# Kernel tuning notes

Hardware: AMD Instinct MI355X
Metric: run time of the kernel (lower is better)

The kernel has to match this reference:

```python
import jax, jax.numpy as jnp
import numpy as np

N_NODES = 50000
N_EDGES = 800000
D_FEAT = 64
NEG_SLOPE = 0.01  # nn.LeakyReLU default


def setup_inputs() -> dict:
    key = jax.random.key(0)
    ks = jax.random.split(key, 8)
    in_feat = jax.random.normal(ks[0], (N_NODES, D_FEAT), dtype=jnp.float32)
    src = jax.random.randint(ks[1], (N_EDGES,), 0, N_NODES, dtype=jnp.int64)
    dst = jax.random.randint(ks[2], (N_EDGES,), 0, N_NODES, dtype=jnp.int64)
    scale = 1.0 / np.sqrt(D_FEAT)
    W1 = jax.random.normal(ks[3], (D_FEAT, D_FEAT), dtype=jnp.float32) * scale
    b1 = jnp.zeros((D_FEAT,), dtype=jnp.float32)
    W2 = jax.random.normal(ks[4], (D_FEAT, D_FEAT), dtype=jnp.float32) * scale
    b2 = jnp.zeros((D_FEAT,), dtype=jnp.float32)
    return {"in_feat": in_feat, "W1": W1, "b1": b1, "W2": W2, "b2": b2,
            "src": src, "dst": dst}


def reference(in_feat, W1, b1, W2, b2, src, dst):
    # Eval-mode GCN: Dropout and DropEdge are identity; per-layer the graph
    # has its self-loops removed (mask src==dst edges) and one canonical
    # self-loop per node re-added. GraphConv uses norm='both':
    #   out = LeakyReLU( (D_in^{-1/2} A D_out^{-1/2} X) W + b )
    N = in_feat.shape[0]
    mask = (src != dst).astype(in_feat.dtype)  # remove_self_loop
    # degrees including the single added self-loop
    out_deg = jax.ops.segment_sum(mask, src, num_segments=N) + 1.0
    in_deg = jax.ops.segment_sum(mask, dst, num_segments=N) + 1.0
    inv_out = jax.lax.rsqrt(out_deg)[:, None]  # [N,1]
    inv_in = jax.lax.rsqrt(in_deg)[:, None]

    def layer(h, W, b):
        hs = h * inv_out                                   # src-side norm
        msg = hs[src] * mask[:, None]                      # gather, drop self-loops
        agg = jax.ops.segment_sum(msg, dst, num_segments=N) + hs  # + self-loop
        agg = agg * inv_in                                 # dst-side norm
        return jax.nn.leaky_relu(agg @ W + b, negative_slope=NEG_SLOPE)

    h = layer(in_feat, W1, b1)
    h = layer(h, W2, b2)
    return h
```

## Files before the change

kernel.cpp:

```cpp
#include <hip/hip_runtime.h>
#include <hip/hip_fp16.h>
#include <stdint.h>

#define D 64
#define NEG_SLOPE 0.01f
#define CAP 64


__global__ void k_zero(int* p, int n) {
    int i = blockIdx.x * blockDim.x + threadIdx.x;
    if (i < n) p[i] = 0;
}

__global__ void k_build(const int* __restrict__ src, const int* __restrict__ dst,
                        int* __restrict__ cnt_in, int* __restrict__ cnt_out,
                        int* __restrict__ colp, int E) {
    int e = blockIdx.x * blockDim.x + threadIdx.x;
    if (e >= E) return;
    int s = src[e], d = dst[e];
    if (s != d) {
        int r = atomicAdd(&cnt_in[d], 1);
        if (r < CAP) colp[(d << 6) + r] = s;
        atomicAdd(&cnt_out[s], 1);
    }
}

__global__ void k_inv(const int* __restrict__ cnt, float* __restrict__ inv, int n2) {
    int i = blockIdx.x * blockDim.x + threadIdx.x;
    if (i < n2) inv[i] = rsqrtf((float)cnt[i] + 1.0f);
}

__global__ void k_prescale(const float* __restrict__ x, const float* __restrict__ inv,
                           __half* __restrict__ y, int total4) {
    int i = blockIdx.x * blockDim.x + threadIdx.x;
    if (i >= total4) return;
    float4 v = reinterpret_cast<const float4*>(x)[i];
    float s = inv[i >> 4];
    __half2* yo = reinterpret_cast<__half2*>(y) + 2 * (size_t)i;
    yo[0] = __half2{__float2half_rn(v.x * s), __float2half_rn(v.y * s)};
    yo[1] = __half2{__float2half_rn(v.z * s), __float2half_rn(v.w * s)};
}

template <bool WRITE_HALF>
__global__ __launch_bounds__(256, 2)
void k_layer(const int* __restrict__ cnt_in, const int* __restrict__ colp,
             const __half* __restrict__ h,
             const float* __restrict__ inv_out, const float* __restrict__ inv_in,
             const float* __restrict__ W, const float* __restrict__ b,
             void* __restrict__ out_, int N) {
    __shared__ float Ws[D * D];
    int tid = threadIdx.x;
    {
        const float4* W4 = reinterpret_cast<const float4*>(W);
        float4* Ws4 = reinterpret_cast<float4*>(Ws);
        for (int i = tid; i < D * D / 4; i += 256) Ws4[i] = W4[i];
    }
    __syncthreads();

    const int lane = tid & 63;
    const int s = lane >> 4;
    const int g = lane & 15;
    const int subbase = lane & 48;
    const int nwaves = gridDim.x * (256 >> 6);
    const int wave0 = (blockIdx.x * 256 + tid) >> 6;
    const int ngroups = (N + 3) >> 2;

    for (int grp = wave0; grp < ngroups; grp += nwaves) {
        const int base = grp * 4;
        const int node = base + s;
        const bool nvalid = node < N;

        int dg = 0;
        if (lane < 4 && base + lane < N) dg = cnt_in[base + lane];
        int deg = __shfl(dg, s);
        deg = deg > CAP ? CAP : deg;
        if (!nvalid) deg = 0;

        int dmax = max(deg, __shfl_xor(deg, 16));
        dmax = max(dmax, __shfl_xor(dmax, 32));

        float a0 = 0.f, a1 = 0.f, a2 = 0.f, a3 = 0.f;
        const int cbase = node << 6;

        for (int cb = 0; cb < dmax; cb += 16) {
            int cnt = deg - cb;  cnt = cnt < 0 ? 0 : (cnt > 16 ? 16 : cnt);
            int cmax = dmax - cb; cmax = cmax > 16 ? 16 : cmax;
            int ci = (g < cnt) ? colp[cbase + cb + g] : 0;
            #pragma unroll
            for (int half = 0; half < 2; ++half) {
                if (half * 8 >= cmax) break;
                uint2 v[8];
                float m[8];
                #pragma unroll
                for (int q = 0; q < 8; ++q) {
                    int it = half * 8 + q;
                    int sn = __shfl(ci, subbase | it);
                    m[q] = (it < cnt) ? 1.f : 0.f;
                    v[q] = *reinterpret_cast<const uint2*>(h + (size_t)sn * D + g * 4);
                }
                #pragma unroll
                for (int q = 0; q < 8; ++q) {
                    float2 f0 = __half22float2(*reinterpret_cast<const __half2*>(&v[q].x));
                    float2 f1 = __half22float2(*reinterpret_cast<const __half2*>(&v[q].y));
                    a0 = fmaf(m[q], f0.x, a0); a1 = fmaf(m[q], f0.y, a1);
                    a2 = fmaf(m[q], f1.x, a2); a3 = fmaf(m[q], f1.y, a3);
                }
            }
        }

        const int nn = nvalid ? node : 0;
        {
            uint2 u = *reinterpret_cast<const uint2*>(h + (size_t)nn * D + g * 4);
            float2 f0 = __half22float2(*reinterpret_cast<const __half2*>(&u.x));
            float2 f1 = __half22float2(*reinterpret_cast<const __half2*>(&u.y));
            float m = nvalid ? 1.f : 0.f;
            a0 = fmaf(m, f0.x, a0); a1 = fmaf(m, f0.y, a1);
            a2 = fmaf(m, f1.x, a2); a3 = fmaf(m, f1.y, a3);
        }
        const float sc = inv_in[nn];
        a0 *= sc; a1 *= sc; a2 *= sc; a3 *= sc;

        const float4 bb = reinterpret_cast<const float4*>(b)[g];
        float r0 = bb.x, r1 = bb.y, r2 = bb.z, r3 = bb.w;
        #pragma unroll
        for (int kq = 0; kq < 16; ++kq) {
            int srcl = subbase | kq;
            float v0 = __shfl(a0, srcl);
            float v1 = __shfl(a1, srcl);
            float v2 = __shfl(a2, srcl);
            float v3 = __shfl(a3, srcl);
            const float4 w0 = *reinterpret_cast<const float4*>(&Ws[(4 * kq + 0) * D + 4 * g]);
            const float4 w1 = *reinterpret_cast<const float4*>(&Ws[(4 * kq + 1) * D + 4 * g]);
            const float4 w2 = *reinterpret_cast<const float4*>(&Ws[(4 * kq + 2) * D + 4 * g]);
            const float4 w3 = *reinterpret_cast<const float4*>(&Ws[(4 * kq + 3) * D + 4 * g]);
            r0 = fmaf(v0, w0.x, r0); r1 = fmaf(v0, w0.y, r1);
            r2 = fmaf(v0, w0.z, r2); r3 = fmaf(v0, w0.w, r3);
            r0 = fmaf(v1, w1.x, r0); r1 = fmaf(v1, w1.y, r1);
            r2 = fmaf(v1, w1.z, r2); r3 = fmaf(v1, w1.w, r3);
            r0 = fmaf(v2, w2.x, r0); r1 = fmaf(v2, w2.y, r1);
            r2 = fmaf(v2, w2.z, r2); r3 = fmaf(v2, w2.w, r3);
            r0 = fmaf(v3, w3.x, r0); r1 = fmaf(v3, w3.y, r1);
            r2 = fmaf(v3, w3.z, r2); r3 = fmaf(v3, w3.w, r3);
        }
        r0 = r0 > 0.f ? r0 : NEG_SLOPE * r0;
        r1 = r1 > 0.f ? r1 : NEG_SLOPE * r1;
        r2 = r2 > 0.f ? r2 : NEG_SLOPE * r2;
        r3 = r3 > 0.f ? r3 : NEG_SLOPE * r3;

        if (nvalid) {
            if (WRITE_HALF) {
                const float so = inv_out[node];
                __half2 o0{__float2half_rn(r0 * so), __float2half_rn(r1 * so)};
                __half2 o1{__float2half_rn(r2 * so), __float2half_rn(r3 * so)};
                uint2 u;
                u.x = *reinterpret_cast<uint32_t*>(&o0);
                u.y = *reinterpret_cast<uint32_t*>(&o1);
                *reinterpret_cast<uint2*>(reinterpret_cast<__half*>(out_) + (size_t)node * D + 4 * g) = u;
            } else {
                float4 o{r0, r1, r2, r3};
                *reinterpret_cast<float4*>(reinterpret_cast<float*>(out_) + (size_t)node * D + 4 * g) = o;
            }
        }
    }
}


extern "C" void kernel_launch(void* const* d_in, const int* in_sizes, int n_in,
                              void* d_out, int out_size, void* d_ws, size_t ws_size,
                              hipStream_t stream) {
    const float* in_feat = (const float*)d_in[0];
    const float* W1      = (const float*)d_in[1];
    const float* b1      = (const float*)d_in[2];
    const float* W2      = (const float*)d_in[3];
    const float* b2      = (const float*)d_in[4];
    const int*   src     = (const int*)d_in[5];
    const int*   dst     = (const int*)d_in[6];

    const int N = in_sizes[0] / D;
    const int E = in_sizes[5];

    float* out = (float*)d_out;
    float* ws  = (float*)d_ws;

    float*  inv_out = ws;
    float*  inv_in  = ws + N;
    int*    cnt     = (int*)(ws + 2 * (size_t)N);
    int*    cnt_out = cnt;
    int*    cnt_in  = cnt + N;
    int*    colp    = cnt + 2 * (size_t)N;
    __half* hh0     = reinterpret_cast<__half*>(((uintptr_t)(colp + (size_t)N * CAP) + 15) & ~(uintptr_t)15);
    __half* h1      = hh0 + (size_t)N * D;

    k_zero<<<(2 * N + 255) / 256, 256, 0, stream>>>(cnt, 2 * N);
    k_build<<<(E + 255) / 256, 256, 0, stream>>>(src, dst, cnt_in, cnt_out, colp, E);
    k_inv<<<(2 * N + 255) / 256, 256, 0, stream>>>(cnt, inv_out, 2 * N);

    k_prescale<<<(N * D / 4 + 255) / 256, 256, 0, stream>>>(in_feat, inv_out, hh0, N * D / 4);

    const int lblocks = min(((N + 3) / 4 * 64 + 255) / 256, 2048);
    k_layer<true ><<<lblocks, 256, 0, stream>>>(cnt_in, colp, hh0, inv_out, inv_in, W1, b1, h1, N);
    k_layer<false><<<lblocks, 256, 0, stream>>>(cnt_in, colp, h1,  inv_out, inv_in, W2, b2, out, N);
}
```

Before: 155.1 us.

## Compute out-degree via LDS-privatized histogram instead of global atomics

Out-degree counting moves out of the edge-building kernel into a separate histogram pass. There are 16 node ranges times 16 edge slices of blocks, and each block counts edges into shared-memory bins. A reduction kernel then sums the slices into cnt_out. The goal is to remove 800k global atomics on cnt_out, at the cost of two extra launches, 16 full reads of src/dst, and a scratch buffer that aliases the half-precision feature area.

```diff
diff --git a/kernel.cpp b/kernel.cpp
--- a/kernel.cpp
+++ b/kernel.cpp
@@ -5,6 +5,9 @@
 #define D 64
 #define NEG_SLOPE 0.01f
 #define CAP 64
+#define HR 16
+#define HS 16
+#define HB 3200
 
 
 __global__ void k_zero(int* p, int n) {
@@ -13,16 +16,47 @@
 }
 
 __global__ void k_build(const int* __restrict__ src, const int* __restrict__ dst,
-                        int* __restrict__ cnt_in, int* __restrict__ cnt_out,
-                        int* __restrict__ colp, int E) {
+                        int* __restrict__ cnt_in, int* __restrict__ colp, int E) {
     int e = blockIdx.x * blockDim.x + threadIdx.x;
     if (e >= E) return;
     int s = src[e], d = dst[e];
     if (s != d) {
         int r = atomicAdd(&cnt_in[d], 1);
         if (r < CAP) colp[(d << 6) + r] = s;
-        atomicAdd(&cnt_out[s], 1);
-    }
+    }
+}
+
+__global__ __launch_bounds__(256)
+void k_hist(const int* __restrict__ src, const int* __restrict__ dst,
+            int* __restrict__ partial, int N, int E, int RB) {
+    __shared__ int bins[HB];
+    const int r  = blockIdx.x & (HR - 1);
+    const int sl = blockIdx.x >> 4;
+    const int lo = r * RB;
+    const int hi = min(N, lo + RB);
+    for (int i = threadIdx.x; i < RB; i += 256) bins[i] = 0;
+    __syncthreads();
+
+    const int per = (E + HS - 1) / HS;
+    const int ebeg = sl * per;
+    const int eend = min(E, ebeg + per);
+    for (int e = ebeg + threadIdx.x; e < eend; e += 256) {
+        int s = src[e];
+        if (s >= lo && s < hi && s != dst[e])
+            atomicAdd(&bins[s - lo], 1);
+    }
+    __syncthreads();
+    for (int i = threadIdx.x; i < hi - lo; i += 256)
+        partial[(size_t)sl * N + lo + i] = bins[i];
+}
+
+__global__ void k_red(const int* __restrict__ partial, int* __restrict__ cnt_out, int N) {
+    int i = blockIdx.x * blockDim.x + threadIdx.x;
+    if (i >= N) return;
+    int sum = 0;
+    #pragma unroll
+    for (int sl = 0; sl < HS; ++sl) sum += partial[(size_t)sl * N + i];
+    cnt_out[i] = sum;
 }
 
 __global__ void k_inv(const int* __restrict__ cnt, float* __restrict__ inv, int n2) {
@@ -178,6 +212,7 @@
 
     const int N = in_sizes[0] / D;
     const int E = in_sizes[5];
+    const int RB = (N + HR - 1) / HR;
 
     float* out = (float*)d_out;
     float* ws  = (float*)d_ws;
@@ -190,9 +225,12 @@
     int*    colp    = cnt + 2 * (size_t)N;
     __half* hh0     = reinterpret_cast<__half*>(((uintptr_t)(colp + (size_t)N * CAP) + 15) & ~(uintptr_t)15);
     __half* h1      = hh0 + (size_t)N * D;
-
-    k_zero<<<(2 * N + 255) / 256, 256, 0, stream>>>(cnt, 2 * N);
-    k_build<<<(E + 255) / 256, 256, 0, stream>>>(src, dst, cnt_in, cnt_out, colp, E);
+    int*    partial = (int*)hh0;
+
+    k_zero<<<(N + 255) / 256, 256, 0, stream>>>(cnt_in, N);
+    k_build<<<(E + 255) / 256, 256, 0, stream>>>(src, dst, cnt_in, colp, E);
+    k_hist<<<HR * HS, 256, 0, stream>>>(src, dst, partial, N, E, RB);
+    k_red<<<(N + 255) / 256, 256, 0, stream>>>(partial, cnt_out, N);
     k_inv<<<(2 * N + 255) / 256, 256, 0, stream>>>(cnt, inv_out, 2 * N);
 
     k_prescale<<<(N * D / 4 + 255) / 256, 256, 0, stream>>>(in_feat, inv_out, hh0, N * D / 4);
```

Result: slower. 243.9 us (+57.3%).

## Prefetch next group's degree, neighbor indices and self row; issue 32 gathers at once

Applied to the files above, without the earlier changes.

The layer kernel now loads the next group's in-degree, its first 32 column indices and the self-feature row one iteration early, so they are in flight while the current group is computed. The first 32 neighbors are fetched with two fully unrolled batches of 16 gathers issued before any accumulation, to raise memory-level parallelism; neighbors beyond 32 use a simple loop. The grid is fixed at 512 blocks so each wave walks several groups and the prefetch has something to overlap with. The cost is much higher register pressure (32 uint2 buffers plus prefetch state), which may cut occupancy, and fewer resident waves to hide latency.

```diff
diff --git a/kernel.cpp b/kernel.cpp
--- a/kernel.cpp
+++ b/kernel.cpp
@@ -61,58 +61,109 @@
     const int s = lane >> 4;
     const int g = lane & 15;
     const int subbase = lane & 48;
-    const int nwaves = gridDim.x * (256 >> 6);
+    const int nwaves = gridDim.x * 4;
     const int wave0 = (blockIdx.x * 256 + tid) >> 6;
     const int ngroups = (N + 3) >> 2;
+    if (wave0 >= ngroups) return;
+
+    const float4 bb4 = reinterpret_cast<const float4*>(b)[g];
+
+    int   p_dg;  int p_c0, p_c1;  uint2 p_self;
+    {
+        const int bb = wave0 * 4;
+        const int nd = bb + s;
+        const int ndc = nd < N ? nd : 0;
+        p_dg = (lane < 4 && bb + lane < N) ? cnt_in[bb + lane] : 0;
+        p_c0 = colp[(ndc << 6) + g];
+        p_c1 = colp[(ndc << 6) + 16 + g];
+        p_self = *reinterpret_cast<const uint2*>(h + (size_t)ndc * D + g * 4);
+    }
 
     for (int grp = wave0; grp < ngroups; grp += nwaves) {
         const int base = grp * 4;
         const int node = base + s;
         const bool nvalid = node < N;
-
-        int dg = 0;
-        if (lane < 4 && base + lane < N) dg = cnt_in[base + lane];
-        int deg = __shfl(dg, s);
+        const int nn = nvalid ? node : 0;
+
+        int deg = __shfl(p_dg, s);
+        if (!nvalid) deg = 0;
         deg = deg > CAP ? CAP : deg;
-        if (!nvalid) deg = 0;
-
         int dmax = max(deg, __shfl_xor(deg, 16));
         dmax = max(dmax, __shfl_xor(dmax, 32));
 
+        int n_dg, n_c0, n_c1; uint2 n_self;
+        {
+            const int gnext = grp + nwaves;
+            const int gg = gnext < ngroups ? gnext : grp;
+            const int bb = gg * 4;
+            const int nd = bb + s;
+            const int ndc = nd < N ? nd : 0;
+            n_dg = (lane < 4 && bb + lane < N) ? cnt_in[bb + lane] : 0;
+            n_c0 = colp[(ndc << 6) + g];
+            n_c1 = colp[(ndc << 6) + 16 + g];
+            n_self = *reinterpret_cast<const uint2*>(h + (size_t)ndc * D + g * 4);
+        }
+
         float a0 = 0.f, a1 = 0.f, a2 = 0.f, a3 = 0.f;
-        const int cbase = node << 6;
-
-        for (int cb = 0; cb < dmax; cb += 16) {
-            int cnt = deg - cb;  cnt = cnt < 0 ? 0 : (cnt > 16 ? 16 : cnt);
+
+        uint2 v[16], w[16];
+        const bool c0on = dmax > 0;
+        const bool c1on = dmax > 16;
+        if (c0on) {
+            #pragma unroll
+            for (int q = 0; q < 16; ++q) {
+                int sn = __shfl(p_c0, subbase | q);
+                sn = (q < deg) ? sn : 0;
+                v[q] = *reinterpret_cast<const uint2*>(h + (size_t)sn * D + g * 4);
+            }
+        }
+        if (c1on) {
+            #pragma unroll
+            for (int q = 0; q < 16; ++q) {
+                int sn = __shfl(p_c1, subbase | q);
+                sn = (16 + q < deg) ? sn : 0;
+                w[q] = *reinterpret_cast<const uint2*>(h + (size_t)sn * D + g * 4);
+            }
+        }
+        if (c0on) {
+            #pragma unroll
+            for (int q = 0; q < 16; ++q) {
+                float m = (q < deg) ? 1.f : 0.f;
+                float2 f0 = __half22float2(*reinterpret_cast<const __half2*>(&v[q].x));
+                float2 f1 = __half22float2(*reinterpret_cast<const __half2*>(&v[q].y));
+                a0 = fmaf(m, f0.x, a0); a1 = fmaf(m, f0.y, a1);
+                a2 = fmaf(m, f1.x, a2); a3 = fmaf(m, f1.y, a3);
+            }
+        }
+        if (c1on) {
+            #pragma unroll
+            for (int q = 0; q < 16; ++q) {
+                float m = (16 + q < deg) ? 1.f : 0.f;
+                float2 f0 = __half22float2(*reinterpret_cast<const __half2*>(&w[q].x));
+                float2 f1 = __half22float2(*reinterpret_cast<const __half2*>(&w[q].y));
+                a0 = fmaf(m, f0.x, a0); a1 = fmaf(m, f0.y, a1);
+                a2 = fmaf(m, f1.x, a2); a3 = fmaf(m, f1.y, a3);
+            }
+        }
+        for (int cb = 32; cb < dmax; cb += 16) {
+            int cnt = deg - cb; cnt = cnt < 0 ? 0 : (cnt > 16 ? 16 : cnt);
             int cmax = dmax - cb; cmax = cmax > 16 ? 16 : cmax;
-            int ci = (g < cnt) ? colp[cbase + cb + g] : 0;
-            #pragma unroll
-            for (int half = 0; half < 2; ++half) {
-                if (half * 8 >= cmax) break;
-                uint2 v[8];
-                float m[8];
-                #pragma unroll
-                for (int q = 0; q < 8; ++q) {
-                    int it = half * 8 + q;
-                    int sn = __shfl(ci, subbase | it);
-                    m[q] = (it < cnt) ? 1.f : 0.f;
-                    v[q] = *reinterpret_cast<const uint2*>(h + (size_t)sn * D + g * 4);
-                }
-                #pragma unroll
-                for (int q = 0; q < 8; ++q) {
-                    float2 f0 = __half22float2(*reinterpret_cast<const __half2*>(&v[q].x));
-                    float2 f1 = __half22float2(*reinterpret_cast<const __half2*>(&v[q].y));
-                    a0 = fmaf(m[q], f0.x, a0); a1 = fmaf(m[q], f0.y, a1);
-                    a2 = fmaf(m[q], f1.x, a2); a3 = fmaf(m[q], f1.y, a3);
-                }
-            }
-        }
-
-        const int nn = nvalid ? node : 0;
+            int ci = (g < cnt) ? colp[(nn << 6) + cb + g] : 0;
+            for (int it = 0; it < cmax; ++it) {
+                int sn = __shfl(ci, subbase | it);
+                sn = (it < cnt) ? sn : 0;
+                float m = (it < cnt) ? 1.f : 0.f;
+                uint2 u = *reinterpret_cast<const uint2*>(h + (size_t)sn * D + g * 4);
+                float2 f0 = __half22float2(*reinterpret_cast<const __half2*>(&u.x));
+                float2 f1 = __half22float2(*reinterpret_cast<const __half2*>(&u.y));
+                a0 = fmaf(m, f0.x, a0); a1 = fmaf(m, f0.y, a1);
+                a2 = fmaf(m, f1.x, a2); a3 = fmaf(m, f1.y, a3);
+            }
+        }
+
         {
-            uint2 u = *reinterpret_cast<const uint2*>(h + (size_t)nn * D + g * 4);
-            float2 f0 = __half22float2(*reinterpret_cast<const __half2*>(&u.x));
-            float2 f1 = __half22float2(*reinterpret_cast<const __half2*>(&u.y));
+            float2 f0 = __half22float2(*reinterpret_cast<const __half2*>(&p_self.x));
+            float2 f1 = __half22float2(*reinterpret_cast<const __half2*>(&p_self.y));
             float m = nvalid ? 1.f : 0.f;
             a0 = fmaf(m, f0.x, a0); a1 = fmaf(m, f0.y, a1);
             a2 = fmaf(m, f1.x, a2); a3 = fmaf(m, f1.y, a3);
@@ -120,8 +171,7 @@
         const float sc = inv_in[nn];
         a0 *= sc; a1 *= sc; a2 *= sc; a3 *= sc;
 
-        const float4 bb = reinterpret_cast<const float4*>(b)[g];
-        float r0 = bb.x, r1 = bb.y, r2 = bb.z, r3 = bb.w;
+        float r0 = bb4.x, r1 = bb4.y, r2 = bb4.z, r3 = bb4.w;
         #pragma unroll
         for (int kq = 0; kq < 16; ++kq) {
             int srcl = subbase | kq;
@@ -161,6 +211,8 @@
                 *reinterpret_cast<float4*>(reinterpret_cast<float*>(out_) + (size_t)node * D + 4 * g) = o;
             }
         }
+
+        p_dg = n_dg; p_c0 = n_c0; p_c1 = n_c1; p_self = n_self;
     }
 }
 
@@ -197,7 +249,7 @@
 
     k_prescale<<<(N * D / 4 + 255) / 256, 256, 0, stream>>>(in_feat, inv_out, hh0, N * D / 4);
 
-    const int lblocks = min(((N + 3) / 4 * 64 + 255) / 256, 2048);
+    const int lblocks = 512;
     k_layer<true ><<<lblocks, 256, 0, stream>>>(cnt_in, colp, hh0, inv_out, inv_in, W1, b1, h1, N);
     k_layer<false><<<lblocks, 256, 0, stream>>>(cnt_in, colp, h1,  inv_out, inv_in, W2, b2, out, N);
 }
```

After: 285.1 us. 83.8% more time.
